# Kernel tuning notes

Measured on AMD Instinct MI355X. Metric: run time of the kernel, lower is better.

Reference implementation:

```python
import jax, jax.numpy as jnp
import numpy as np

N_NODES = 20000
N_EDGES = 640000
CHANNELS = 128
EDGE_ATTR_DIM = 1


def setup_inputs() -> dict:
    key = jax.random.key(0)
    ks = jax.random.split(key, 10)
    C, E, N = CHANNELS, N_EDGES, N_NODES
    x_a = jax.random.normal(ks[0], (N, C), dtype=jnp.float32)
    edge_index = jax.random.randint(ks[1], (2, E), 0, N, dtype=jnp.int64)
    edge_attr = jax.random.uniform(ks[2], (E, EDGE_ATTR_DIM), dtype=jnp.float32)
    # Linear params (stored as [in, out]); scaled like torch default init
    g_in = 2 * C + EDGE_ATTR_DIM
    g_w = jax.random.uniform(ks[3], (g_in, C), jnp.float32, -1, 1) / np.sqrt(g_in)
    g_b = jax.random.uniform(ks[4], (C,), jnp.float32, -1, 1) / np.sqrt(g_in)
    f_w = jax.random.uniform(ks[5], (2 * C, C), jnp.float32, -1, 1) / np.sqrt(2 * C)
    f_b = jax.random.uniform(ks[6], (C,), jnp.float32, -1, 1) / np.sqrt(2 * C)
    cls_w = jax.random.uniform(ks[7], (C, 1), jnp.float32, -1, 1) / np.sqrt(C)
    cls_b = jax.random.uniform(ks[8], (1,), jnp.float32, -1, 1) / np.sqrt(C)
    return {"x_a": x_a, "edge_index": edge_index, "edge_attr": edge_attr,
            "g_w": g_w, "g_b": g_b, "f_w": f_w, "f_b": f_b,
            "cls_w": cls_w, "cls_b": cls_b}


def reference(x_a, edge_index, edge_attr, g_w, g_b, f_w, f_b, cls_w, cls_b):
    # PyG MessagePassing (flow source_to_target): x_j = x[src], x_i = x[dst]
    src = edge_index[0]
    dst = edge_index[1]
    N = x_a.shape[0]
    # message: g([x_i, x_j, e_ij])  -> [E, C]
    z_ij = jnp.concatenate([x_a[dst], x_a[src], edge_attr], axis=-1)
    msg = z_ij @ g_w + g_b
    # aggregate: scatter-mean over destination nodes (empty nodes -> 0)
    sums = jax.ops.segment_sum(msg, dst, num_segments=N)
    cnt = jax.ops.segment_sum(jnp.ones((dst.shape[0], 1), x_a.dtype), dst,
                              num_segments=N)
    aggr = sums / jnp.maximum(cnt, 1.0)
    # update: f([x, aggr])
    h = jnp.concatenate([x_a, aggr], axis=-1) @ f_w + f_b
    # classifier + sigmoid + threshold
    probs = jax.nn.sigmoid(h @ cls_w + cls_b)
    y = probs > 0.5
    return (y, probs)
```

## Files before the change

### kernel.cpp

```cpp
#include <hip/hip_runtime.h>
#include <math.h>

#define NNODES 20000
#define NEDGES 640000
#define C 128

#define NB1 256
#define BT 1024

#define NB 128

#define CNT_SHIFT 26
#define EDGE_BIAS (1 << 19)
#define SUM_MASK 0x03FFFFFFu

__global__ void __launch_bounds__(BT)
k_node(const float* __restrict__ x,
       const float* __restrict__ g_w, const float* __restrict__ g_b,
       const float* __restrict__ f_w, const float* __restrict__ f_b,
       const float* __restrict__ cls_w, const float* __restrict__ cls_b,
       float* __restrict__ xu, float* __restrict__ xp,
       float* __restrict__ r, float* __restrict__ scal)
{
    __shared__ float csh[C], vsh[C], ush[C], psh[C], qsh[C];
    const int tid = threadIdx.x;
    const int pair = tid >> 2;
    const int prt  = tid & 3;
    const int k = pair & 127;
    const int h = pair >> 7;

    if (tid < C) csh[tid] = cls_w[tid];
    __syncthreads();

    const float4* fw4 = (const float4*)f_w;
    const float4* gw4 = (const float4*)g_w;
    const float4* cs4 = (const float4*)csh;

    {
        const float4* row = fw4 + (size_t)(h * C + k) * (C / 4) + prt * 8;
        const float4* cc  = cs4 + prt * 8;
        float s = 0.f;
        #pragma unroll
        for (int j = 0; j < 8; ++j) {
            float4 a = row[j], c = cc[j];
            s += a.x * c.x + a.y * c.y + a.z * c.z + a.w * c.w;
        }
        s += __shfl_down(s, 2);
        s += __shfl_down(s, 1);
        if (prt == 0) { if (h == 0) ush[k] = s; else vsh[k] = s; }
    }
    __syncthreads();

    const float4* vs4 = (const float4*)vsh;
    {
        const float4* row = gw4 + (size_t)(h * C + k) * (C / 4) + prt * 8;
        const float4* vv  = vs4 + prt * 8;
        float s = 0.f;
        #pragma unroll
        for (int j = 0; j < 8; ++j) {
            float4 a = row[j], c = vv[j];
            s += a.x * c.x + a.y * c.y + a.z * c.z + a.w * c.w;
        }
        s += __shfl_down(s, 2);
        s += __shfl_down(s, 1);
        if (prt == 0) { if (h == 0) psh[k] = s; else qsh[k] = s; }
    }
    __syncthreads();

    if (blockIdx.x == 0 && tid < 192) {
        int w = tid >> 6, lane = tid & 63;
        float a, b;
        if (w == 0)      { a = g_b[lane] * vsh[lane];          b = g_b[lane + 64] * vsh[lane + 64]; }
        else if (w == 1) { a = g_w[256 * C + lane] * vsh[lane]; b = g_w[256 * C + lane + 64] * vsh[lane + 64]; }
        else             { a = f_b[lane] * csh[lane];          b = f_b[lane + 64] * csh[lane + 64]; }
        float s = a + b;
        for (int off = 32; off > 0; off >>= 1) s += __shfl_down(s, off);
        if (lane == 0) scal[w] = (w == 2) ? s + cls_b[0] : s;
    }

    {
        int w = tid >> 6, lane = tid & 63;
        int gwave = blockIdx.x * (BT / 64) + w;
        float2 uu = ((const float2*)ush)[lane];
        float2 pp = ((const float2*)psh)[lane];
        float2 qq = ((const float2*)qsh)[lane];

        for (int n = gwave; n < NNODES; n += NB1 * (BT / 64)) {
            float2 xx = ((const float2*)(x + (size_t)n * C))[lane];
            float du = xx.x * uu.x + xx.y * uu.y;
            float dp = xx.x * pp.x + xx.y * pp.y;
            float dq = xx.x * qq.x + xx.y * qq.y;
            for (int off = 32; off > 0; off >>= 1) {
                du += __shfl_down(du, off);
                dp += __shfl_down(dp, off);
                dq += __shfl_down(dq, off);
            }
            if (lane == 0) { xu[n] = du; xp[n] = dp; r[n] = dq; }
        }
    }
}

__global__ void __launch_bounds__(BT)
k_edge(const int* __restrict__ ei, const float* __restrict__ attr,
       const float* __restrict__ r, const float* __restrict__ scal,
       unsigned int* __restrict__ part)
{
    __shared__ unsigned int lacc[NNODES];
    int tid = threadIdx.x;

    uint4* l4 = (uint4*)lacc;
    for (int i = tid; i < NNODES / 4; i += BT) l4[i] = make_uint4(0u, 0u, 0u, 0u);
    __syncthreads();

    float gev = scal[1];
    for (int e = blockIdx.x * BT + tid; e < NEDGES; e += NB * BT) {
        int s = ei[e];
        int d = ei[NEDGES + e];
        float t = r[s] + attr[e] * gev;
        int fix = __float2int_rn(t * 65536.0f);
        atomicAdd(&lacc[d], (1u << CNT_SHIFT) + (unsigned int)(fix + EDGE_BIAS));
    }
    __syncthreads();

    uint4* mp4 = (uint4*)(part + (size_t)blockIdx.x * NNODES);
    for (int i = tid; i < NNODES / 4; i += BT) mp4[i] = l4[i];
}

__global__ void __launch_bounds__(256)
k_final(const float* __restrict__ xu, const float* __restrict__ xp,
        const unsigned int* __restrict__ part,
        const float* __restrict__ scal, float* __restrict__ out)
{
    int n = blockIdx.x * 256 + threadIdx.x;
    if (n >= NNODES) return;

    int sumfix = 0, cnt = 0;
    const unsigned int* pb = part + n;
    #pragma unroll 16
    for (int b = 0; b < NB; ++b) {
        unsigned int v = pb[(size_t)b * NNODES];
        int c = (int)(v >> CNT_SHIFT);
        cnt += c;
        sumfix += (int)(v & SUM_MASK) - (c << 19);
    }

    float sacc = (float)sumfix * (1.0f / 65536.0f);
    float cmax = fmaxf((float)cnt, 1.0f);
    float cfac = (cnt > 0) ? 1.0f : 0.0f;
    float logit = xu[n] + cfac * (xp[n] + scal[0]) + sacc / cmax + scal[2];
    float pr = 1.0f / (1.0f + expf(-logit));
    out[n] = (pr > 0.5f) ? 1.0f : 0.0f;
    out[NNODES + n] = pr;
}

extern "C" void kernel_launch(void* const* d_in, const int* in_sizes, int n_in,
                              void* d_out, int out_size, void* d_ws, size_t ws_size,
                              hipStream_t stream) {
    const float* x_a       = (const float*)d_in[0];
    const int*   ei        = (const int*)d_in[1];
    const float* edge_attr = (const float*)d_in[2];
    const float* g_w       = (const float*)d_in[3];
    const float* g_b       = (const float*)d_in[4];
    const float* f_w       = (const float*)d_in[5];
    const float* f_b       = (const float*)d_in[6];
    const float* cls_w     = (const float*)d_in[7];
    const float* cls_b     = (const float*)d_in[8];
    float* out = (float*)d_out;

    unsigned int* part = (unsigned int*)d_ws;
    float* xu   = (float*)d_ws + (size_t)NB * NNODES;
    float* xp   = xu + NNODES;
    float* r    = xp + NNODES;
    float* scal = r + NNODES;

    k_node<<<NB1, BT, 0, stream>>>(x_a, g_w, g_b, f_w, f_b, cls_w, cls_b,
                                   xu, xp, r, scal);

    k_edge<<<NB, BT, 0, stream>>>(ei, edge_attr, r, scal, part);

    k_final<<<(NNODES + 255) / 256, 256, 0, stream>>>(xu, xp, part, scal, out);
}
```

Baseline: 104.1 us.

## Split edge scatter by destination half and parallelize final partial reduction

The edge kernel now launches twice as many blocks. Each block handles one contiguous edge chunk but only the destination nodes in one half of the node range, so its shared-memory accumulator is halved and more blocks can be resident. The final kernel splits the 128 partial reads for each node across 4 lanes and combines them with shuffles, which gives more parallelism for the memory-bound reduction. The cost is that every edge's indices are read twice, once per node half, which doubles index traffic.

```diff
diff --git a/kernel.cpp b/kernel.cpp
--- a/kernel.cpp
+++ b/kernel.cpp
@@ -8,7 +8,9 @@
 #define NB1 256
 #define BT 1024
 
-#define NB 128
+#define NCHUNK 128
+#define EPC (NEDGES / NCHUNK)
+#define HALFN (NNODES / 2)
 
 #define CNT_SHIFT 26
 #define EDGE_BIAS (1 << 19)
@@ -105,25 +107,33 @@
        const float* __restrict__ r, const float* __restrict__ scal,
        unsigned int* __restrict__ part)
 {
-    __shared__ unsigned int lacc[NNODES];
-    int tid = threadIdx.x;
+    __shared__ unsigned int lacc[HALFN];
+    const int tid = threadIdx.x;
+    const int chunk = blockIdx.x & (NCHUNK - 1);
+    const int h     = blockIdx.x >> 7;
+    const int nbase = h * HALFN;
 
     uint4* l4 = (uint4*)lacc;
-    for (int i = tid; i < NNODES / 4; i += BT) l4[i] = make_uint4(0u, 0u, 0u, 0u);
-    __syncthreads();
-
-    float gev = scal[1];
-    for (int e = blockIdx.x * BT + tid; e < NEDGES; e += NB * BT) {
+    for (int i = tid; i < HALFN / 4; i += BT) l4[i] = make_uint4(0u, 0u, 0u, 0u);
+    __syncthreads();
+
+    const float gev = scal[1];
+    const int ebase = chunk * EPC;
+    for (int i = tid; i < EPC; i += BT) {
+        int e = ebase + i;
         int s = ei[e];
         int d = ei[NEDGES + e];
-        float t = r[s] + attr[e] * gev;
-        int fix = __float2int_rn(t * 65536.0f);
-        atomicAdd(&lacc[d], (1u << CNT_SHIFT) + (unsigned int)(fix + EDGE_BIAS));
-    }
-    __syncthreads();
-
-    uint4* mp4 = (uint4*)(part + (size_t)blockIdx.x * NNODES);
-    for (int i = tid; i < NNODES / 4; i += BT) mp4[i] = l4[i];
+        unsigned int idx = (unsigned int)(d - nbase);
+        if (idx < HALFN) {
+            float t = r[s] + attr[e] * gev;
+            int fix = __float2int_rn(t * 65536.0f);
+            atomicAdd(&lacc[idx], (1u << CNT_SHIFT) + (unsigned int)(fix + EDGE_BIAS));
+        }
+    }
+    __syncthreads();
+
+    uint4* mp4 = (uint4*)(part + (size_t)(chunk * 2 + h) * HALFN);
+    for (int i = tid; i < HALFN / 4; i += BT) mp4[i] = l4[i];
 }
 
 __global__ void __launch_bounds__(256)
@@ -131,26 +141,38 @@
         const unsigned int* __restrict__ part,
         const float* __restrict__ scal, float* __restrict__ out)
 {
-    int n = blockIdx.x * 256 + threadIdx.x;
-    if (n >= NNODES) return;
+    int t = threadIdx.x;
+    int quad = t >> 2;
+    int prt  = t & 3;
+    int n = blockIdx.x * 64 + quad;
 
     int sumfix = 0, cnt = 0;
-    const unsigned int* pb = part + n;
-    #pragma unroll 16
-    for (int b = 0; b < NB; ++b) {
-        unsigned int v = pb[(size_t)b * NNODES];
-        int c = (int)(v >> CNT_SHIFT);
-        cnt += c;
-        sumfix += (int)(v & SUM_MASK) - (c << 19);
-    }
-
-    float sacc = (float)sumfix * (1.0f / 65536.0f);
-    float cmax = fmaxf((float)cnt, 1.0f);
-    float cfac = (cnt > 0) ? 1.0f : 0.0f;
-    float logit = xu[n] + cfac * (xp[n] + scal[0]) + sacc / cmax + scal[2];
-    float pr = 1.0f / (1.0f + expf(-logit));
-    out[n] = (pr > 0.5f) ? 1.0f : 0.0f;
-    out[NNODES + n] = pr;
+    if (n < NNODES) {
+        int h   = (n >= HALFN) ? 1 : 0;
+        int idx = n - h * HALFN;
+        const unsigned int* pb = part + (size_t)((prt * 32) * 2 + h) * HALFN + idx;
+        #pragma unroll
+        for (int b = 0; b < NCHUNK / 4; ++b) {
+            unsigned int v = pb[(size_t)b * 2 * HALFN];
+            int c = (int)(v >> CNT_SHIFT);
+            cnt += c;
+            sumfix += (int)(v & SUM_MASK) - (c << 19);
+        }
+    }
+    sumfix += __shfl_down(sumfix, 1);
+    sumfix += __shfl_down(sumfix, 2);
+    cnt    += __shfl_down(cnt, 1);
+    cnt    += __shfl_down(cnt, 2);
+
+    if (prt == 0 && n < NNODES) {
+        float sacc = (float)sumfix * (1.0f / 65536.0f);
+        float cmax = fmaxf((float)cnt, 1.0f);
+        float cfac = (cnt > 0) ? 1.0f : 0.0f;
+        float logit = xu[n] + cfac * (xp[n] + scal[0]) + sacc / cmax + scal[2];
+        float pr = 1.0f / (1.0f + expf(-logit));
+        out[n] = (pr > 0.5f) ? 1.0f : 0.0f;
+        out[NNODES + n] = pr;
+    }
 }
 
 extern "C" void kernel_launch(void* const* d_in, const int* in_sizes, int n_in,
@@ -168,7 +190,7 @@
     float* out = (float*)d_out;
 
     unsigned int* part = (unsigned int*)d_ws;
-    float* xu   = (float*)d_ws + (size_t)NB * NNODES;
+    float* xu   = (float*)d_ws + (size_t)NCHUNK * NNODES;
     float* xp   = xu + NNODES;
     float* r    = xp + NNODES;
     float* scal = r + NNODES;
@@ -176,7 +198,7 @@
     k_node<<<NB1, BT, 0, stream>>>(x_a, g_w, g_b, f_w, f_b, cls_w, cls_b,
                                    xu, xp, r, scal);
 
-    k_edge<<<NB, BT, 0, stream>>>(ei, edge_attr, r, scal, part);
-
-    k_final<<<(NNODES + 255) / 256, 256, 0, stream>>>(xu, xp, part, scal, out);
-}
+    k_edge<<<NCHUNK * 2, BT, 0, stream>>>(ei, edge_attr, r, scal, part);
+
+    k_final<<<(NNODES + 63) / 64, 256, 0, stream>>>(xu, xp, part, scal, out);
+}
```

Result: no change. 102.2 us (-1.9%).
